# Kernel optimization log

Measured on AMD Instinct MI355X. Metric: run time of the kernel, lower is better.

Reference implementation:

```python
import jax, jax.numpy as jnp
import numpy as np

D_MODEL = 256
N_HEADS = 8
HEAD_DIM = D_MODEL // N_HEADS
EPS = 1e-6


def setup_inputs() -> dict:
    key = jax.random.key(0)
    ks = jax.random.split(key, 12)
    B, L, S = 8, 8192, 8192
    scale = 1.0 / np.sqrt(D_MODEL)
    inp = {
        "queries": jax.random.normal(ks[0], (B, L, D_MODEL), jnp.float32),
        "keys": jax.random.normal(ks[1], (B, S, D_MODEL), jnp.float32),
        "values": jax.random.normal(ks[2], (B, S, D_MODEL), jnp.float32),
        "query_masks": jnp.ones((B, L), jnp.float32),
        "key_masks": jnp.ones((B, S), jnp.float32),
        # nn.Linear params (torch layout: W [out,in], y = x @ W.T + b)
        "Wq": jax.random.normal(ks[3], (D_MODEL, D_MODEL), jnp.float32) * scale,
        "bq": jax.random.normal(ks[4], (D_MODEL,), jnp.float32) * scale,
        "Wk": jax.random.normal(ks[5], (D_MODEL, D_MODEL), jnp.float32) * scale,
        "bk": jax.random.normal(ks[6], (D_MODEL,), jnp.float32) * scale,
        "Wv": jax.random.normal(ks[7], (D_MODEL, D_MODEL), jnp.float32) * scale,
        "bv": jax.random.normal(ks[8], (D_MODEL,), jnp.float32) * scale,
        "Wm": jax.random.normal(ks[9], (D_MODEL, D_MODEL), jnp.float32) * scale,
        "bm": jax.random.normal(ks[10], (D_MODEL,), jnp.float32) * scale,
    }
    return inp


def _feature_map(x):
    return jax.nn.elu(x) + 1.0


def reference(queries, keys, values, query_masks, key_masks,
              Wq, bq, Wk, bk, Wv, bv, Wm, bm):
    B, L, D = queries.shape
    S = keys.shape[1]
    H, hd = N_HEADS, HEAD_DIM

    q = (queries @ Wq.T + bq).reshape(B, L, H, hd)
    k = (keys @ Wk.T + bk).reshape(B, S, H, hd)
    v = (values @ Wv.T + bv).reshape(B, S, H, hd)

    Q = _feature_map(q) * query_masks[:, :, None, None]
    K = _feature_map(k) * key_masks[:, :, None, None]
    v = v * key_masks[:, :, None, None]

    # KV: [B,H,hd_v(m),hd_k(d)]
    KV = jnp.einsum("nshd,nshm->nhmd", K, v)
    Z = 1.0 / (jnp.einsum("nlhd,nhd->nlh", Q, K.sum(axis=1)) + EPS)
    V = jnp.einsum("nlhd,nhmd,nlh->nlhm", Q, KV, Z)
    return V.reshape(B, L, D) @ Wm.T + bm
```

## Files before the change

kernel.cpp:

```cpp
#include <hip/hip_runtime.h>
#include <math.h>


#define B_ 8
#define S_ 8192
#define D_ 256
#define H_ 8
#define EPS_ 1e-6f

typedef short short8 __attribute__((ext_vector_type(8)));
typedef float f32x16 __attribute__((ext_vector_type(16)));

#define KA_K 0
#define KA_V 32768
#define KA_M 65536
#define KA_BYTES 66048
#define KB_Q 0
#define KB_O 32768
#define KB_M 65536
#define KB_S 66048
#define KB_BQ 67072
#define KB_BYTES 68096

static __device__ __forceinline__ unsigned short f2bf(float f) {
  union { float f; unsigned u; } v; v.f = f;
  return (unsigned short)((v.u + 0x7fffu + ((v.u >> 16) & 1u)) >> 16);
}
static __device__ __forceinline__ unsigned pack2(float a, float b) {
  return (unsigned)f2bf(a) | ((unsigned)f2bf(b) << 16);
}

static __device__ __forceinline__ void stage_issue(const float* __restrict__ src,
                                                   int tid, float4* R) {
  const float4* s4 = (const float4*)src;
#pragma unroll
  for (int i = 0; i < 16; ++i) R[i] = s4[i * 256 + tid];
}
static __device__ __forceinline__ void stage_write(char* __restrict__ dst,
                                                   int tid, const float4* R) {
  const int w = tid >> 6, lane = tid & 63, g = lane >> 1, j = lane & 1;
#pragma unroll
  for (int i = 0; i < 16; ++i) {
    const int tok = 4 * i + w;
    *(ushort4*)(dst + ((g * 64 + (tok ^ (g & 31))) * 16 + j * 8)) =
        make_ushort4(f2bf(R[i].x), f2bf(R[i].y), f2bf(R[i].z), f2bf(R[i].w));
  }
}

static __device__ __forceinline__ short8 mk_frag(unsigned w00, unsigned w01,
                                                 unsigned w10, unsigned w11, int kg) {
  unsigned a0 = kg ? w10 : w00, a1 = kg ? w11 : w01;
  unsigned s0 = kg ? w00 : w10, s1 = kg ? w01 : w11;
  unsigned r0 = __shfl_xor(s0, 32), r1 = __shfl_xor(s1, 32);
  union { unsigned u[4]; short8 s8; } f;
  f.u[0] = kg ? r0 : a0; f.u[1] = kg ? r1 : a1;
  f.u[2] = kg ? a0 : r0; f.u[3] = kg ? a1 : r1;
  return f.s8;
}

template <bool XOR>
static __device__ __forceinline__ void gemm_std(const char* __restrict__ ldsX,
                                                const short8* __restrict__ Wf,
                                                int w, int lo, int kg, f32x16 acc[2][2]) {
#pragma unroll
  for (int a = 0; a < 2; ++a)
#pragma unroll
    for (int c = 0; c < 2; ++c)
#pragma unroll
      for (int i = 0; i < 16; ++i) acc[a][c][i] = 0.f;
#pragma unroll 4
  for (int ks = 0; ks < 16; ++ks) {
    const int g = 2 * ks + kg;
    short8 af[2], bf[2];
#pragma unroll
    for (int mt = 0; mt < 2; ++mt) {
      int tok = mt * 32 + lo;
      if (XOR) tok ^= (g & 31);
      af[mt] = *(const short8*)(ldsX + (g * 64 + tok) * 16);
    }
#pragma unroll
    for (int nt = 0; nt < 2; ++nt) bf[nt] = Wf[g * 256 + w * 64 + nt * 32 + lo];
#pragma unroll
    for (int mt = 0; mt < 2; ++mt)
#pragma unroll
      for (int nt = 0; nt < 2; ++nt)
        acc[mt][nt] = __builtin_amdgcn_mfma_f32_32x32x16_bf16(af[mt], bf[nt],
                                                              acc[mt][nt], 0, 0, 0);
  }
}

static __device__ __forceinline__ void gemm_flip(const char* __restrict__ ldsX,
                                                 const short8* __restrict__ Wf,
                                                 int w, int lo, int kg, f32x16 acc[2][2]) {
#pragma unroll
  for (int a = 0; a < 2; ++a)
#pragma unroll
    for (int c = 0; c < 2; ++c)
#pragma unroll
      for (int i = 0; i < 16; ++i) acc[a][c][i] = 0.f;
#pragma unroll 4
  for (int ks = 0; ks < 16; ++ks) {
    const int g = 2 * ks + kg;
    short8 aw[2], bx[2];
#pragma unroll
    for (int At = 0; At < 2; ++At) aw[At] = Wf[g * 256 + w * 64 + At * 32 + lo];
#pragma unroll
    for (int Bt = 0; Bt < 2; ++Bt)
      bx[Bt] = *(const short8*)(ldsX + (g * 64 + ((Bt * 32 + lo) ^ (g & 31))) * 16);
#pragma unroll
    for (int At = 0; At < 2; ++At)
#pragma unroll
      for (int Bt = 0; Bt < 2; ++Bt)
        acc[At][Bt] = __builtin_amdgcn_mfma_f32_32x32x16_bf16(aw[At], bx[Bt],
                                                              acc[At][Bt], 0, 0, 0);
  }
}

__global__ void kPrep(const float* __restrict__ Wq, const float* __restrict__ Wk,
                      const float* __restrict__ Wv, const float* __restrict__ Wm,
                      unsigned short* __restrict__ Wf) {
  int idx = blockIdx.x * 256 + threadIdx.x;
  int wsel = idx >> 13, g = (idx >> 8) & 31, o = idx & 255;
  const float* W = wsel == 0 ? Wq : wsel == 1 ? Wk : wsel == 2 ? Wv : Wm;
  const float* p = W + o * 256 + g * 8;
  *(ushort4*)(Wf + (size_t)idx * 8) =
      make_ushort4(f2bf(p[0]), f2bf(p[1]), f2bf(p[2]), f2bf(p[3]));
  *(ushort4*)(Wf + (size_t)idx * 8 + 4) =
      make_ushort4(f2bf(p[4]), f2bf(p[5]), f2bf(p[6]), f2bf(p[7]));
}

__global__ void __launch_bounds__(256, 2)
kA(const float* __restrict__ keys, const float* __restrict__ values,
   const float* __restrict__ kmask,
   const float* __restrict__ bk, const float* __restrict__ bv,
   const short8* __restrict__ WfK, const short8* __restrict__ WfV,
   float* __restrict__ kvpart, float* __restrict__ kspart,
   float* __restrict__ KV, float* __restrict__ Ksum, int use_atomic) {
  extern __shared__ char lds[];
  char* ldsK = lds + KA_K;
  char* ldsV = lds + KA_V;
  float* ldsM = (float*)(lds + KA_M);
  const int tid = threadIdx.x, w = tid >> 6, lane = tid & 63, lo = lane & 31, kg = lane >> 5;
  const int blk = blockIdx.x, b = blockIdx.y;
  const size_t base = ((size_t)b * S_ + blk * 128) * D_;

  const float bk0 = bk[w * 64 + lo], bk1 = bk[w * 64 + 32 + lo];
  const float bv0 = bv[w * 64 + lo], bv1 = bv[w * 64 + 32 + lo];

  f32x16 kvacc[2];
#pragma unroll
  for (int hh = 0; hh < 2; ++hh)
#pragma unroll
    for (int i = 0; i < 16; ++i) kvacc[hh][i] = 0.f;
  float ks0 = 0.f, ks1 = 0.f;

  float4 RK[16], RV[16];
  stage_issue(keys + base, tid, RK);
  stage_issue(values + base, tid, RV);
  if (tid < 128) ldsM[tid] = kmask[(size_t)b * S_ + blk * 128 + tid];
  stage_write(ldsK, tid, RK);

#pragma unroll
  for (int it = 0; it < 2; ++it) {
    __syncthreads();
    f32x16 acc[2][2];
    gemm_std<true>(ldsK, WfK, w, lo, kg, acc);

    unsigned Wk_[2][2][4][2];
#pragma unroll
    for (int mt = 0; mt < 2; ++mt)
#pragma unroll
      for (int nt = 0; nt < 2; ++nt) {
        const float bias = nt ? bk1 : bk0;
#pragma unroll
        for (int q = 0; q < 4; ++q) {
          float vv[4];
#pragma unroll
          for (int c = 0; c < 4; ++c) {
            const int tok = it * 64 + 32 * mt + 8 * q + 4 * kg + c;
            float f = acc[mt][nt][4 * q + c] + bias;
            f = f > 0.f ? f + 1.f : __expf(f);
            f *= ldsM[tok];
            if (nt == 0) ks0 += f; else ks1 += f;
            vv[c] = f;
          }
          Wk_[mt][nt][q][0] = pack2(vv[0], vv[1]);
          Wk_[mt][nt][q][1] = pack2(vv[2], vv[3]);
        }
      }
    short8 kf[2][4];
#pragma unroll
    for (int nt = 0; nt < 2; ++nt)
#pragma unroll
      for (int mt = 0; mt < 2; ++mt)
#pragma unroll
        for (int sel = 0; sel < 2; ++sel)
          kf[nt][2 * mt + sel] = mk_frag(Wk_[mt][nt][2 * sel][0], Wk_[mt][nt][2 * sel][1],
                                         Wk_[mt][nt][2 * sel + 1][0], Wk_[mt][nt][2 * sel + 1][1], kg);

    stage_write(ldsV, tid, RV);
    if (it == 0) stage_issue(keys + base + 64 * D_, tid, RK);
    __syncthreads();

    gemm_std<true>(ldsV, WfV, w, lo, kg, acc);
    unsigned Wv_[2][2][4][2];
#pragma unroll
    for (int mt = 0; mt < 2; ++mt)
#pragma unroll
      for (int nt = 0; nt < 2; ++nt) {
        const float bias = nt ? bv1 : bv0;
#pragma unroll
        for (int q = 0; q < 4; ++q) {
          float vv[4];
#pragma unroll
          for (int c = 0; c < 4; ++c) {
            const int tok = it * 64 + 32 * mt + 8 * q + 4 * kg + c;
            vv[c] = (acc[mt][nt][4 * q + c] + bias) * ldsM[tok];
          }
          Wv_[mt][nt][q][0] = pack2(vv[0], vv[1]);
          Wv_[mt][nt][q][1] = pack2(vv[2], vv[3]);
        }
      }
    short8 vf[2][4];
#pragma unroll
    for (int nt = 0; nt < 2; ++nt)
#pragma unroll
      for (int mt = 0; mt < 2; ++mt)
#pragma unroll
        for (int sel = 0; sel < 2; ++sel)
          vf[nt][2 * mt + sel] = mk_frag(Wv_[mt][nt][2 * sel][0], Wv_[mt][nt][2 * sel][1],
                                         Wv_[mt][nt][2 * sel + 1][0], Wv_[mt][nt][2 * sel + 1][1], kg);
    if (it == 0) stage_issue(values + base + 64 * D_, tid, RV);

#pragma unroll
    for (int hh = 0; hh < 2; ++hh)
#pragma unroll
      for (int tg = 0; tg < 4; ++tg)
        kvacc[hh] = __builtin_amdgcn_mfma_f32_32x32x16_bf16(kf[hh][tg], vf[hh][tg],
                                                            kvacc[hh], 0, 0, 0);
    if (it == 0) stage_write(ldsK, tid, RK);
  }

  const float tot0 = ks0 + __shfl_xor(ks0, 32);
  const float tot1 = ks1 + __shfl_xor(ks1, 32);
  if (use_atomic) {
    atomicAdd(&Ksum[b * 256 + w * 64 + kg * 32 + lo], kg ? tot1 : tot0);
#pragma unroll
    for (int hh = 0; hh < 2; ++hh) {
      const int h = 2 * w + hh;
#pragma unroll
      for (int r = 0; r < 16; ++r) {
        const int d = (r & 3) + 8 * (r >> 2) + 4 * kg;
        atomicAdd(&KV[(((size_t)b * H_ + h) * 32 + lo) * 32 + d], kvacc[hh][r]);
      }
    }
  } else {
    kspart[((size_t)b * 64 + blk) * 256 + w * 64 + kg * 32 + lo] = kg ? tot1 : tot0;
#pragma unroll
    for (int hh = 0; hh < 2; ++hh) {
      const int h = 2 * w + hh;
      float* dst = kvpart + ((size_t)b * 64 + blk) * 8192 + ((h * 2 + kg) * 16) * 32 + lo;
#pragma unroll
      for (int r = 0; r < 16; ++r) dst[r * 32] = kvacc[hh][r];
    }
  }
}

__global__ void kR(const float* __restrict__ kvpart, const float* __restrict__ kspart,
                   float* __restrict__ KV, float* __restrict__ Ksum) {
  int idx = blockIdx.x * 256 + threadIdx.x;
  if (idx < 65536) {
    int b = idx >> 13, r2 = idx & 8191;
    int h = r2 >> 10, kg2 = (r2 >> 9) & 1, rr = (r2 >> 5) & 15, m = r2 & 31;
    const float* p = kvpart + (size_t)b * 64 * 8192 + r2;
    float s = 0.f;
#pragma unroll 8
    for (int j = 0; j < 64; ++j) s += p[(size_t)j * 8192];
    int d = (rr & 3) + 4 * kg2 + 8 * (rr >> 2);
    KV[(((size_t)b * H_ + h) * 32 + m) * 32 + d] = s;
  } else if (idx < 67584) {
    int t = idx - 65536;
    int b = t >> 8, o = t & 255;
    const float* p = kspart + (size_t)b * 64 * 256 + o;
    float s = 0.f;
#pragma unroll 8
    for (int j = 0; j < 64; ++j) s += p[j * 256];
    Ksum[t] = s;
  }
}

__global__ void __launch_bounds__(256, 2)
kB(const float* __restrict__ queries, const float* __restrict__ qmask,
   const float* __restrict__ bq, const float* __restrict__ bm,
   const short8* __restrict__ WfQ, const short8* __restrict__ WfM,
   const float* __restrict__ KV, const float* __restrict__ Ksum,
   float* __restrict__ out) {
  extern __shared__ char lds[];
  char* ldsQ = lds + KB_Q;
  char* ldsO = lds + KB_O;
  float* ldsM = (float*)(lds + KB_M);
  float* ldsS = (float*)(lds + KB_S);
  float* ldsBq = (float*)(lds + KB_BQ);
  const int tid = threadIdx.x, w = tid >> 6, lane = tid & 63, lo = lane & 31, kg = lane >> 5;
  const int blk = blockIdx.x, b = blockIdx.y;
  const size_t base = ((size_t)b * S_ + blk * 128) * D_;

  ldsS[tid] = Ksum[b * 256 + tid];
  ldsBq[tid] = bq[tid];
  if (tid < 128) ldsM[tid] = qmask[(size_t)b * S_ + blk * 128 + tid];
  const float bm0 = bm[w * 64 + lo], bm1 = bm[w * 64 + 32 + lo];

  short8 kvf[2][2];
#pragma unroll
  for (int hh = 0; hh < 2; ++hh)
#pragma unroll
    for (int ksd = 0; ksd < 2; ++ksd) {
      const float* p = KV + (((size_t)b * H_ + 2 * w + hh) * 32 + lo) * 32 + ksd * 16 + kg * 8;
      float4 x0 = *(const float4*)p, x1 = *(const float4*)(p + 4);
      union { unsigned u[4]; short8 s8; } t;
      t.u[0] = pack2(x0.x, x0.y); t.u[1] = pack2(x0.z, x0.w);
      t.u[2] = pack2(x1.x, x1.y); t.u[3] = pack2(x1.z, x1.w);
      kvf[hh][ksd] = t.s8;
    }

  float4 RQ[16];
  stage_issue(queries + base, tid, RQ);
  stage_write(ldsQ, tid, RQ);

#pragma unroll
  for (int it = 0; it < 2; ++it) {
    __syncthreads();
    f32x16 qa[2][2];
    gemm_flip(ldsQ, WfQ, w, lo, kg, qa);
    if (it == 0) stage_issue(queries + base + 64 * D_, tid, RQ);

    unsigned Wq_[2][2][4][2];
    float inv_[2][2];
#pragma unroll
    for (int At = 0; At < 2; ++At) {
      float kss[4][4], bql[4][4];
#pragma unroll
      for (int q = 0; q < 4; ++q)
#pragma unroll
        for (int c = 0; c < 4; ++c) {
          const int o = w * 64 + At * 32 + 8 * q + 4 * kg + c;
          kss[q][c] = ldsS[o];
          bql[q][c] = ldsBq[o];
        }
#pragma unroll
      for (int Bt = 0; Bt < 2; ++Bt) {
        const float qm = ldsM[it * 64 + Bt * 32 + lo];
        float z = 0.f;
#pragma unroll
        for (int q = 0; q < 4; ++q) {
          float vv[4];
#pragma unroll
          for (int c = 0; c < 4; ++c) {
            float f = qa[At][Bt][4 * q + c] + bql[q][c];
            f = f > 0.f ? f + 1.f : __expf(f);
            f *= qm;
            z += f * kss[q][c];
            vv[c] = f;
          }
          Wq_[At][Bt][q][0] = pack2(vv[0], vv[1]);
          Wq_[At][Bt][q][1] = pack2(vv[2], vv[3]);
        }
        const float zf = z + __shfl_xor(z, 32);
        inv_[At][Bt] = 1.0f / (zf + EPS_);
      }
    }

#pragma unroll
    for (int hh = 0; hh < 2; ++hh) {
      const int h = 2 * w + hh;
#pragma unroll
      for (int Bt = 0; Bt < 2; ++Bt) {
        f32x16 pn;
#pragma unroll
        for (int i = 0; i < 16; ++i) pn[i] = 0.f;
#pragma unroll
        for (int ksd = 0; ksd < 2; ++ksd) {
          short8 qf = mk_frag(Wq_[hh][Bt][2 * ksd][0], Wq_[hh][Bt][2 * ksd][1],
                              Wq_[hh][Bt][2 * ksd + 1][0], Wq_[hh][Bt][2 * ksd + 1][1], kg);
          pn = __builtin_amdgcn_mfma_f32_32x32x16_bf16(kvf[hh][ksd], qf, pn, 0, 0, 0);
        }
        const float inv = inv_[hh][Bt];
        const int tok = Bt * 32 + lo;
#pragma unroll
        for (int q = 0; q < 4; ++q)
          *(ushort4*)(ldsO + ((h * 4 + q) * 64 + tok) * 16 + kg * 8) =
              make_ushort4(f2bf(pn[4 * q + 0] * inv), f2bf(pn[4 * q + 1] * inv),
                           f2bf(pn[4 * q + 2] * inv), f2bf(pn[4 * q + 3] * inv));
      }
    }
    __syncthreads();

    f32x16 oa[2][2];
    gemm_std<false>(ldsO, WfM, w, lo, kg, oa);
    if (it == 0) stage_write(ldsQ, tid, RQ);

    const int t0 = blk * 128 + it * 64;
#pragma unroll
    for (int mt = 0; mt < 2; ++mt)
#pragma unroll
      for (int nt = 0; nt < 2; ++nt) {
        const float bias = nt ? bm1 : bm0;
        const int o = w * 64 + nt * 32 + lo;
        float* dst = out + ((size_t)b * S_ + t0 + 32 * mt) * D_ + o;
#pragma unroll
        for (int r = 0; r < 16; ++r) {
          const int tok = (r & 3) + 8 * (r >> 2) + 4 * kg;
          dst[(size_t)tok * D_] = oa[mt][nt][r] + bias;
        }
      }
  }
}

extern "C" void kernel_launch(void* const* d_in, const int* in_sizes, int n_in,
                              void* d_out, int out_size, void* d_ws, size_t ws_size,
                              hipStream_t stream) {
  const float* queries = (const float*)d_in[0];
  const float* keys    = (const float*)d_in[1];
  const float* values  = (const float*)d_in[2];
  const float* qmask   = (const float*)d_in[3];
  const float* kmask   = (const float*)d_in[4];
  const float* Wq = (const float*)d_in[5];
  const float* bq = (const float*)d_in[6];
  const float* Wk = (const float*)d_in[7];
  const float* bk = (const float*)d_in[8];
  const float* Wv = (const float*)d_in[9];
  const float* bv = (const float*)d_in[10];
  const float* Wm = (const float*)d_in[11];
  const float* bm = (const float*)d_in[12];
  float* out = (float*)d_out;

  char* ws = (char*)d_ws;
  unsigned short* Wf = (unsigned short*)ws;
  float* KV   = (float*)(ws + 524288);
  float* Ksum = (float*)(ws + 786432);
  float* kvpart = (float*)(ws + 1048576);
  float* kspart = (float*)(ws + 1048576 + 16777216);
  const size_t need = 1048576 + 16777216 + 524288;
  const int use_atomic = (ws_size < need) ? 1 : 0;

  hipFuncSetAttribute(reinterpret_cast<const void*>(kA),
                      hipFuncAttributeMaxDynamicSharedMemorySize, KA_BYTES);
  hipFuncSetAttribute(reinterpret_cast<const void*>(kB),
                      hipFuncAttributeMaxDynamicSharedMemorySize, KB_BYTES);

  kPrep<<<128, 256, 0, stream>>>(Wq, Wk, Wv, Wm, Wf);
  if (use_atomic) hipMemsetAsync(ws + 524288, 0, 262144 + 8192, stream);

  const short8* Wf8 = (const short8*)Wf;
  kA<<<dim3(64, B_), 256, KA_BYTES, stream>>>(keys, values, kmask, bk, bv,
      Wf8 + (size_t)1 * 8192, Wf8 + (size_t)2 * 8192, kvpart, kspart, KV, Ksum, use_atomic);
  if (!use_atomic) kR<<<264, 256, 0, stream>>>(kvpart, kspart, KV, Ksum);
  kB<<<dim3(64, B_), 256, KB_BYTES, stream>>>(queries, qmask, bq, bm,
      Wf8, Wf8 + (size_t)3 * 8192, KV, Ksum, out);
}
```

Baseline: 316.8 us.

## Stage fp32 tiles via direct global-to-LDS loads and shrink per-block token tiles

Both projection kernels now load fp32 input rows straight into LDS with global_load_lds into a swizzled layout, then convert to bf16 with v_cvt_pk_bf16_f32 when reading MFMA fragments. This replaces the register-staged load, convert and store path. kA now works on 32-token tiles with a single LDS buffer shared by keys and values over four iterations. kB handles 32 tokens per block with four times as many blocks, and LDS is cut so that three blocks fit per CU. The aim is to save VGPRs and staging instructions and to raise occupancy, at the cost of less prefetch overlap between tiles and smaller MFMA tiles per wave.

After: 370.1 us. 1.17x slower.

```diff
diff --git a/kernel.cpp b/kernel.cpp
--- a/kernel.cpp
+++ b/kernel.cpp
@@ -11,16 +11,15 @@
 typedef short short8 __attribute__((ext_vector_type(8)));
 typedef float f32x16 __attribute__((ext_vector_type(16)));
 
-#define KA_K 0
-#define KA_V 32768
-#define KA_M 65536
-#define KA_BYTES 66048
+#define KA_X 0
+#define KA_M 32768
+#define KA_BYTES 33280
 #define KB_Q 0
 #define KB_O 32768
-#define KB_M 65536
-#define KB_S 66048
-#define KB_BQ 67072
-#define KB_BYTES 68096
+#define KB_M 49152
+#define KB_S 49280
+#define KB_BQ 50304
+#define KB_BYTES 51328
 
 static __device__ __forceinline__ unsigned short f2bf(float f) {
   union { float f; unsigned u; } v; v.f = f;
@@ -29,22 +28,41 @@
 static __device__ __forceinline__ unsigned pack2(float a, float b) {
   return (unsigned)f2bf(a) | ((unsigned)f2bf(b) << 16);
 }
-
-static __device__ __forceinline__ void stage_issue(const float* __restrict__ src,
-                                                   int tid, float4* R) {
-  const float4* s4 = (const float4*)src;
-#pragma unroll
-  for (int i = 0; i < 16; ++i) R[i] = s4[i * 256 + tid];
-}
-static __device__ __forceinline__ void stage_write(char* __restrict__ dst,
-                                                   int tid, const float4* R) {
-  const int w = tid >> 6, lane = tid & 63, g = lane >> 1, j = lane & 1;
-#pragma unroll
-  for (int i = 0; i < 16; ++i) {
-    const int tok = 4 * i + w;
-    *(ushort4*)(dst + ((g * 64 + (tok ^ (g & 31))) * 16 + j * 8)) =
-        make_ushort4(f2bf(R[i].x), f2bf(R[i].y), f2bf(R[i].z), f2bf(R[i].w));
-  }
+static __device__ __forceinline__ unsigned cvt_pk(float a, float b) {
+  unsigned r;
+  asm("v_cvt_pk_bf16_f32 %0, %1, %2" : "=v"(r) : "v"(a), "v"(b));
+  return r;
+}
+
+typedef __attribute__((address_space(1))) const void GV;
+typedef __attribute__((address_space(3))) void LV;
+static __device__ __forceinline__ void gll16(const void* gp, void* lp) {
+  __builtin_amdgcn_global_load_lds((GV*)gp, (LV*)lp, 16, 0, 0);
+}
+
+static __device__ __forceinline__ void issue_tile(const float* __restrict__ src,
+                                                  char* __restrict__ buf,
+                                                  int w, int lane) {
+#pragma unroll
+  for (int i = 0; i < 8; ++i) {
+    const int r = w * 8 + i;
+    const float* gp = src + r * 256 + ((lane ^ (r & 15)) << 2);
+    gll16((const void*)gp, (void*)(buf + r * 1024));
+  }
+}
+
+static __device__ __forceinline__ short8 ld_frag_f32(const char* __restrict__ ldsX,
+                                                     int row, int g) {
+  const int s0 = (g * 2) ^ (row & 15);
+  const int s1 = (g * 2 + 1) ^ (row & 15);
+  float4 a = *(const float4*)(ldsX + row * 1024 + s0 * 16);
+  float4 b = *(const float4*)(ldsX + row * 1024 + s1 * 16);
+  union { unsigned u[4]; short8 s8; } t;
+  t.u[0] = cvt_pk(a.x, a.y);
+  t.u[1] = cvt_pk(a.z, a.w);
+  t.u[2] = cvt_pk(b.x, b.y);
+  t.u[3] = cvt_pk(b.z, b.w);
+  return t.s8;
 }
 
 static __device__ __forceinline__ short8 mk_frag(unsigned w00, unsigned w01,
@@ -56,64 +74,6 @@
   f.u[0] = kg ? r0 : a0; f.u[1] = kg ? r1 : a1;
   f.u[2] = kg ? a0 : r0; f.u[3] = kg ? a1 : r1;
   return f.s8;
-}
-
-template <bool XOR>
-static __device__ __forceinline__ void gemm_std(const char* __restrict__ ldsX,
-                                                const short8* __restrict__ Wf,
-                                                int w, int lo, int kg, f32x16 acc[2][2]) {
-#pragma unroll
-  for (int a = 0; a < 2; ++a)
-#pragma unroll
-    for (int c = 0; c < 2; ++c)
-#pragma unroll
-      for (int i = 0; i < 16; ++i) acc[a][c][i] = 0.f;
-#pragma unroll 4
-  for (int ks = 0; ks < 16; ++ks) {
-    const int g = 2 * ks + kg;
-    short8 af[2], bf[2];
-#pragma unroll
-    for (int mt = 0; mt < 2; ++mt) {
-      int tok = mt * 32 + lo;
-      if (XOR) tok ^= (g & 31);
-      af[mt] = *(const short8*)(ldsX + (g * 64 + tok) * 16);
-    }
-#pragma unroll
-    for (int nt = 0; nt < 2; ++nt) bf[nt] = Wf[g * 256 + w * 64 + nt * 32 + lo];
-#pragma unroll
-    for (int mt = 0; mt < 2; ++mt)
-#pragma unroll
-      for (int nt = 0; nt < 2; ++nt)
-        acc[mt][nt] = __builtin_amdgcn_mfma_f32_32x32x16_bf16(af[mt], bf[nt],
-                                                              acc[mt][nt], 0, 0, 0);
-  }
-}
-
-static __device__ __forceinline__ void gemm_flip(const char* __restrict__ ldsX,
-                                                 const short8* __restrict__ Wf,
-                                                 int w, int lo, int kg, f32x16 acc[2][2]) {
-#pragma unroll
-  for (int a = 0; a < 2; ++a)
-#pragma unroll
-    for (int c = 0; c < 2; ++c)
-#pragma unroll
-      for (int i = 0; i < 16; ++i) acc[a][c][i] = 0.f;
-#pragma unroll 4
-  for (int ks = 0; ks < 16; ++ks) {
-    const int g = 2 * ks + kg;
-    short8 aw[2], bx[2];
-#pragma unroll
-    for (int At = 0; At < 2; ++At) aw[At] = Wf[g * 256 + w * 64 + At * 32 + lo];
-#pragma unroll
-    for (int Bt = 0; Bt < 2; ++Bt)
-      bx[Bt] = *(const short8*)(ldsX + (g * 64 + ((Bt * 32 + lo) ^ (g & 31))) * 16);
-#pragma unroll
-    for (int At = 0; At < 2; ++At)
-#pragma unroll
-      for (int Bt = 0; Bt < 2; ++Bt)
-        acc[At][Bt] = __builtin_amdgcn_mfma_f32_32x32x16_bf16(aw[At], bx[Bt],
-                                                              acc[At][Bt], 0, 0, 0);
-  }
 }
 
 __global__ void kPrep(const float* __restrict__ Wq, const float* __restrict__ Wk,
@@ -129,7 +89,7 @@
       make_ushort4(f2bf(p[4]), f2bf(p[5]), f2bf(p[6]), f2bf(p[7]));
 }
 
-__global__ void __launch_bounds__(256, 2)
+__global__ void __launch_bounds__(256, 3)
 kA(const float* __restrict__ keys, const float* __restrict__ values,
    const float* __restrict__ kmask,
    const float* __restrict__ bk, const float* __restrict__ bv,
@@ -137,8 +97,7 @@
    float* __restrict__ kvpart, float* __restrict__ kspart,
    float* __restrict__ KV, float* __restrict__ Ksum, int use_atomic) {
   extern __shared__ char lds[];
-  char* ldsK = lds + KA_K;
-  char* ldsV = lds + KA_V;
+  char* bufX = lds + KA_X;
   float* ldsM = (float*)(lds + KA_M);
   const int tid = threadIdx.x, w = tid >> 6, lane = tid & 63, lo = lane & 31, kg = lane >> 5;
   const int blk = blockIdx.x, b = blockIdx.y;
@@ -154,91 +113,101 @@
     for (int i = 0; i < 16; ++i) kvacc[hh][i] = 0.f;
   float ks0 = 0.f, ks1 = 0.f;
 
-  float4 RK[16], RV[16];
-  stage_issue(keys + base, tid, RK);
-  stage_issue(values + base, tid, RV);
   if (tid < 128) ldsM[tid] = kmask[(size_t)b * S_ + blk * 128 + tid];
-  stage_write(ldsK, tid, RK);
-
-#pragma unroll
-  for (int it = 0; it < 2; ++it) {
+  issue_tile(keys + base, bufX, w, lane);
+
+#pragma unroll 1
+  for (int it = 0; it < 4; ++it) {
     __syncthreads();
-    f32x16 acc[2][2];
-    gemm_std<true>(ldsK, WfK, w, lo, kg, acc);
-
-    unsigned Wk_[2][2][4][2];
-#pragma unroll
-    for (int mt = 0; mt < 2; ++mt)
-#pragma unroll
-      for (int nt = 0; nt < 2; ++nt) {
-        const float bias = nt ? bk1 : bk0;
-#pragma unroll
-        for (int q = 0; q < 4; ++q) {
-          float vv[4];
-#pragma unroll
-          for (int c = 0; c < 4; ++c) {
-            const int tok = it * 64 + 32 * mt + 8 * q + 4 * kg + c;
-            float f = acc[mt][nt][4 * q + c] + bias;
-            f = f > 0.f ? f + 1.f : __expf(f);
-            f *= ldsM[tok];
-            if (nt == 0) ks0 += f; else ks1 += f;
-            vv[c] = f;
-          }
-          Wk_[mt][nt][q][0] = pack2(vv[0], vv[1]);
-          Wk_[mt][nt][q][1] = pack2(vv[2], vv[3]);
+
+    f32x16 acc[2];
+#pragma unroll
+    for (int nt = 0; nt < 2; ++nt)
+#pragma unroll
+      for (int i = 0; i < 16; ++i) acc[nt][i] = 0.f;
+#pragma unroll 4
+    for (int ks = 0; ks < 16; ++ks) {
+      const int g = 2 * ks + kg;
+      short8 af = ld_frag_f32(bufX, lo, g);
+      short8 b0 = WfK[g * 256 + w * 64 + lo];
+      short8 b1 = WfK[g * 256 + w * 64 + 32 + lo];
+      acc[0] = __builtin_amdgcn_mfma_f32_32x32x16_bf16(af, b0, acc[0], 0, 0, 0);
+      acc[1] = __builtin_amdgcn_mfma_f32_32x32x16_bf16(af, b1, acc[1], 0, 0, 0);
+    }
+    __syncthreads();
+    issue_tile(values + base + (size_t)it * 32 * D_, bufX, w, lane);
+
+    unsigned Wk_[2][4][2];
+#pragma unroll
+    for (int nt = 0; nt < 2; ++nt) {
+      const float bias = nt ? bk1 : bk0;
+#pragma unroll
+      for (int q = 0; q < 4; ++q) {
+        float vv[4];
+#pragma unroll
+        for (int c = 0; c < 4; ++c) {
+          const int tok = 8 * q + 4 * kg + c;
+          float f = acc[nt][4 * q + c] + bias;
+          f = f > 0.f ? f + 1.f : __expf(f);
+          f *= ldsM[it * 32 + tok];
+          if (nt == 0) ks0 += f; else ks1 += f;
+          vv[c] = f;
         }
+        Wk_[nt][q][0] = pack2(vv[0], vv[1]);
+        Wk_[nt][q][1] = pack2(vv[2], vv[3]);
       }
-    short8 kf[2][4];
+    }
+    short8 kf[2][2];
 #pragma unroll
     for (int nt = 0; nt < 2; ++nt)
 #pragma unroll
-      for (int mt = 0; mt < 2; ++mt)
-#pragma unroll
-        for (int sel = 0; sel < 2; ++sel)
-          kf[nt][2 * mt + sel] = mk_frag(Wk_[mt][nt][2 * sel][0], Wk_[mt][nt][2 * sel][1],
-                                         Wk_[mt][nt][2 * sel + 1][0], Wk_[mt][nt][2 * sel + 1][1], kg);
-
-    stage_write(ldsV, tid, RV);
-    if (it == 0) stage_issue(keys + base + 64 * D_, tid, RK);
+      for (int sel = 0; sel < 2; ++sel)
+        kf[nt][sel] = mk_frag(Wk_[nt][2 * sel][0], Wk_[nt][2 * sel][1],
+                              Wk_[nt][2 * sel + 1][0], Wk_[nt][2 * sel + 1][1], kg);
+
     __syncthreads();
 
-    gemm_std<true>(ldsV, WfV, w, lo, kg, acc);
-    unsigned Wv_[2][2][4][2];
-#pragma unroll
-    for (int mt = 0; mt < 2; ++mt)
-#pragma unroll
-      for (int nt = 0; nt < 2; ++nt) {
-        const float bias = nt ? bv1 : bv0;
-#pragma unroll
-        for (int q = 0; q < 4; ++q) {
-          float vv[4];
-#pragma unroll
-          for (int c = 0; c < 4; ++c) {
-            const int tok = it * 64 + 32 * mt + 8 * q + 4 * kg + c;
-            vv[c] = (acc[mt][nt][4 * q + c] + bias) * ldsM[tok];
-          }
-          Wv_[mt][nt][q][0] = pack2(vv[0], vv[1]);
-          Wv_[mt][nt][q][1] = pack2(vv[2], vv[3]);
+#pragma unroll
+    for (int nt = 0; nt < 2; ++nt)
+#pragma unroll
+      for (int i = 0; i < 16; ++i) acc[nt][i] = 0.f;
+#pragma unroll 4
+    for (int ks = 0; ks < 16; ++ks) {
+      const int g = 2 * ks + kg;
+      short8 af = ld_frag_f32(bufX, lo, g);
+      short8 b0 = WfV[g * 256 + w * 64 + lo];
+      short8 b1 = WfV[g * 256 + w * 64 + 32 + lo];
+      acc[0] = __builtin_amdgcn_mfma_f32_32x32x16_bf16(af, b0, acc[0], 0, 0, 0);
+      acc[1] = __builtin_amdgcn_mfma_f32_32x32x16_bf16(af, b1, acc[1], 0, 0, 0);
+    }
+    __syncthreads();
+    if (it < 3) issue_tile(keys + base + (size_t)(it + 1) * 32 * D_, bufX, w, lane);
+
+    unsigned Wv_[2][4][2];
+#pragma unroll
+    for (int nt = 0; nt < 2; ++nt) {
+      const float bias = nt ? bv1 : bv0;
+#pragma unroll
+      for (int q = 0; q < 4; ++q) {
+        float vv[4];
+#pragma unroll
+        for (int c = 0; c < 4; ++c) {
+          const int tok = 8 * q + 4 * kg + c;
+          vv[c] = (acc[nt][4 * q + c] + bias) * ldsM[it * 32 + tok];
         }
+        Wv_[nt][q][0] = pack2(vv[0], vv[1]);
+        Wv_[nt][q][1] = pack2(vv[2], vv[3]);
       }
-    short8 vf[2][4];
-#pragma unroll
-    for (int nt = 0; nt < 2; ++nt)
-#pragma unroll
-      for (int mt = 0; mt < 2; ++mt)
-#pragma unroll
-        for (int sel = 0; sel < 2; ++sel)
-          vf[nt][2 * mt + sel] = mk_frag(Wv_[mt][nt][2 * sel][0], Wv_[mt][nt][2 * sel][1],
-                                         Wv_[mt][nt][2 * sel + 1][0], Wv_[mt][nt][2 * sel + 1][1], kg);
-    if (it == 0) stage_issue(values + base + 64 * D_, tid, RV);
-
+    }
 #pragma unroll
     for (int hh = 0; hh < 2; ++hh)
 #pragma unroll
-      for (int tg = 0; tg < 4; ++tg)
-        kvacc[hh] = __builtin_amdgcn_mfma_f32_32x32x16_bf16(kf[hh][tg], vf[hh][tg],
+      for (int sel = 0; sel < 2; ++sel) {
+        short8 vf = mk_frag(Wv_[hh][2 * sel][0], Wv_[hh][2 * sel][1],
+                            Wv_[hh][2 * sel + 1][0], Wv_[hh][2 * sel + 1][1], kg);
+        kvacc[hh] = __builtin_amdgcn_mfma_f32_32x32x16_bf16(kf[hh][sel], vf,
                                                             kvacc[hh], 0, 0, 0);
-    if (it == 0) stage_write(ldsK, tid, RK);
+      }
   }
 
   const float tot0 = ks0 + __shfl_xor(ks0, 32);
@@ -289,25 +258,27 @@
   }
 }
 
-__global__ void __launch_bounds__(256, 2)
+__global__ void __launch_bounds__(256, 3)
 kB(const float* __restrict__ queries, const float* __restrict__ qmask,
    const float* __restrict__ bq, const float* __restrict__ bm,
    const short8* __restrict__ WfQ, const short8* __restrict__ WfM,
    const float* __restrict__ KV, const float* __restrict__ Ksum,
    float* __restrict__ out) {
   extern __shared__ char lds[];
-  char* ldsQ = lds + KB_Q;
+  char* bufQ = lds + KB_Q;
   char* ldsO = lds + KB_O;
   float* ldsM = (float*)(lds + KB_M);
   float* ldsS = (float*)(lds + KB_S);
   float* ldsBq = (float*)(lds + KB_BQ);
   const int tid = threadIdx.x, w = tid >> 6, lane = tid & 63, lo = lane & 31, kg = lane >> 5;
   const int blk = blockIdx.x, b = blockIdx.y;
-  const size_t base = ((size_t)b * S_ + blk * 128) * D_;
+  const size_t base = ((size_t)b * S_ + blk * 32) * D_;
+
+  issue_tile(queries + base, bufQ, w, lane);
 
   ldsS[tid] = Ksum[b * 256 + tid];
   ldsBq[tid] = bq[tid];
-  if (tid < 128) ldsM[tid] = qmask[(size_t)b * S_ + blk * 128 + tid];
+  if (tid < 32) ldsM[tid] = qmask[(size_t)b * S_ + blk * 32 + tid];
   const float bm0 = bm[w * 64 + lo], bm1 = bm[w * 64 + 32 + lo];
 
   short8 kvf[2][2];
@@ -323,96 +294,93 @@
       kvf[hh][ksd] = t.s8;
     }
 
-  float4 RQ[16];
-  stage_issue(queries + base, tid, RQ);
-  stage_write(ldsQ, tid, RQ);
-
-#pragma unroll
-  for (int it = 0; it < 2; ++it) {
-    __syncthreads();
-    f32x16 qa[2][2];
-    gemm_flip(ldsQ, WfQ, w, lo, kg, qa);
-    if (it == 0) stage_issue(queries + base + 64 * D_, tid, RQ);
-
-    unsigned Wq_[2][2][4][2];
-    float inv_[2][2];
-#pragma unroll
-    for (int At = 0; At < 2; ++At) {
-      float kss[4][4], bql[4][4];
-#pragma unroll
-      for (int q = 0; q < 4; ++q)
-#pragma unroll
-        for (int c = 0; c < 4; ++c) {
-          const int o = w * 64 + At * 32 + 8 * q + 4 * kg + c;
-          kss[q][c] = ldsS[o];
-          bql[q][c] = ldsBq[o];
-        }
-#pragma unroll
-      for (int Bt = 0; Bt < 2; ++Bt) {
-        const float qm = ldsM[it * 64 + Bt * 32 + lo];
-        float z = 0.f;
-#pragma unroll
-        for (int q = 0; q < 4; ++q) {
-          float vv[4];
-#pragma unroll
-          for (int c = 0; c < 4; ++c) {
-            float f = qa[At][Bt][4 * q + c] + bql[q][c];
-            f = f > 0.f ? f + 1.f : __expf(f);
-            f *= qm;
-            z += f * kss[q][c];
-            vv[c] = f;
-          }
-          Wq_[At][Bt][q][0] = pack2(vv[0], vv[1]);
-          Wq_[At][Bt][q][1] = pack2(vv[2], vv[3]);
-        }
-        const float zf = z + __shfl_xor(z, 32);
-        inv_[At][Bt] = 1.0f / (zf + EPS_);
+  __syncthreads();
+
+  f32x16 qa[2];
+#pragma unroll
+  for (int At = 0; At < 2; ++At)
+#pragma unroll
+    for (int i = 0; i < 16; ++i) qa[At][i] = 0.f;
+#pragma unroll 4
+  for (int ks = 0; ks < 16; ++ks) {
+    const int g = 2 * ks + kg;
+    short8 a0 = WfQ[g * 256 + w * 64 + lo];
+    short8 a1 = WfQ[g * 256 + w * 64 + 32 + lo];
+    short8 bx = ld_frag_f32(bufQ, lo, g);
+    qa[0] = __builtin_amdgcn_mfma_f32_32x32x16_bf16(a0, bx, qa[0], 0, 0, 0);
+    qa[1] = __builtin_amdgcn_mfma_f32_32x32x16_bf16(a1, bx, qa[1], 0, 0, 0);
+  }
+
+  unsigned Wq_[2][4][2];
+  float inv_[2];
+  const float qm = ldsM[lo];
+#pragma unroll
+  for (int At = 0; At < 2; ++At) {
+    float z = 0.f;
+#pragma unroll
+    for (int q = 0; q < 4; ++q) {
+      float vv[4];
+#pragma unroll
+      for (int c = 0; c < 4; ++c) {
+        const int o = w * 64 + At * 32 + 8 * q + 4 * kg + c;
+        float f = qa[At][4 * q + c] + ldsBq[o];
+        f = f > 0.f ? f + 1.f : __expf(f);
+        f *= qm;
+        z += f * ldsS[o];
+        vv[c] = f;
       }
-    }
-
-#pragma unroll
-    for (int hh = 0; hh < 2; ++hh) {
-      const int h = 2 * w + hh;
-#pragma unroll
-      for (int Bt = 0; Bt < 2; ++Bt) {
-        f32x16 pn;
-#pragma unroll
-        for (int i = 0; i < 16; ++i) pn[i] = 0.f;
-#pragma unroll
-        for (int ksd = 0; ksd < 2; ++ksd) {
-          short8 qf = mk_frag(Wq_[hh][Bt][2 * ksd][0], Wq_[hh][Bt][2 * ksd][1],
-                              Wq_[hh][Bt][2 * ksd + 1][0], Wq_[hh][Bt][2 * ksd + 1][1], kg);
-          pn = __builtin_amdgcn_mfma_f32_32x32x16_bf16(kvf[hh][ksd], qf, pn, 0, 0, 0);
-        }
-        const float inv = inv_[hh][Bt];
-        const int tok = Bt * 32 + lo;
-#pragma unroll
-        for (int q = 0; q < 4; ++q)
-          *(ushort4*)(ldsO + ((h * 4 + q) * 64 + tok) * 16 + kg * 8) =
-              make_ushort4(f2bf(pn[4 * q + 0] * inv), f2bf(pn[4 * q + 1] * inv),
-                           f2bf(pn[4 * q + 2] * inv), f2bf(pn[4 * q + 3] * inv));
-      }
-    }
-    __syncthreads();
-
-    f32x16 oa[2][2];
-    gemm_std<false>(ldsO, WfM, w, lo, kg, oa);
-    if (it == 0) stage_write(ldsQ, tid, RQ);
-
-    const int t0 = blk * 128 + it * 64;
-#pragma unroll
-    for (int mt = 0; mt < 2; ++mt)
-#pragma unroll
-      for (int nt = 0; nt < 2; ++nt) {
-        const float bias = nt ? bm1 : bm0;
-        const int o = w * 64 + nt * 32 + lo;
-        float* dst = out + ((size_t)b * S_ + t0 + 32 * mt) * D_ + o;
-#pragma unroll
-        for (int r = 0; r < 16; ++r) {
-          const int tok = (r & 3) + 8 * (r >> 2) + 4 * kg;
-          dst[(size_t)tok * D_] = oa[mt][nt][r] + bias;
-        }
-      }
+      Wq_[At][q][0] = pack2(vv[0], vv[1]);
+      Wq_[At][q][1] = pack2(vv[2], vv[3]);
+    }
+    const float zf = z + __shfl_xor(z, 32);
+    inv_[At] = 1.0f / (zf + EPS_);
+  }
+
+#pragma unroll
+  for (int hh = 0; hh < 2; ++hh) {
+    const int h = 2 * w + hh;
+    f32x16 pn;
+#pragma unroll
+    for (int i = 0; i < 16; ++i) pn[i] = 0.f;
+#pragma unroll
+    for (int ksd = 0; ksd < 2; ++ksd) {
+      short8 qf = mk_frag(Wq_[hh][2 * ksd][0], Wq_[hh][2 * ksd][1],
+                          Wq_[hh][2 * ksd + 1][0], Wq_[hh][2 * ksd + 1][1], kg);
+      pn = __builtin_amdgcn_mfma_f32_32x32x16_bf16(kvf[hh][ksd], qf, pn, 0, 0, 0);
+    }
+    const float inv = inv_[hh];
+#pragma unroll
+    for (int q = 0; q < 4; ++q)
+      *(ushort4*)(ldsO + ((h * 4 + q) * 32 + lo) * 16 + kg * 8) =
+          make_ushort4(f2bf(pn[4 * q + 0] * inv), f2bf(pn[4 * q + 1] * inv),
+                       f2bf(pn[4 * q + 2] * inv), f2bf(pn[4 * q + 3] * inv));
+  }
+  __syncthreads();
+
+  f32x16 oa[2];
+#pragma unroll
+  for (int nt = 0; nt < 2; ++nt)
+#pragma unroll
+    for (int i = 0; i < 16; ++i) oa[nt][i] = 0.f;
+#pragma unroll 4
+  for (int ks = 0; ks < 16; ++ks) {
+    const int g = 2 * ks + kg;
+    short8 av = *(const short8*)(ldsO + (g * 32 + lo) * 16);
+    short8 b0 = WfM[g * 256 + w * 64 + lo];
+    short8 b1 = WfM[g * 256 + w * 64 + 32 + lo];
+    oa[0] = __builtin_amdgcn_mfma_f32_32x32x16_bf16(av, b0, oa[0], 0, 0, 0);
+    oa[1] = __builtin_amdgcn_mfma_f32_32x32x16_bf16(av, b1, oa[1], 0, 0, 0);
+  }
+#pragma unroll
+  for (int nt = 0; nt < 2; ++nt) {
+    const float bias = nt ? bm1 : bm0;
+    const int o = w * 64 + nt * 32 + lo;
+    float* dst = out + ((size_t)b * S_ + blk * 32) * D_ + o;
+#pragma unroll
+    for (int r = 0; r < 16; ++r) {
+      const int tok = (r & 3) + 8 * (r >> 2) + 4 * kg;
+      dst[(size_t)tok * D_] = oa[nt][r] + bias;
+    }
   }
 }
 
@@ -443,18 +411,18 @@
   const size_t need = 1048576 + 16777216 + 524288;
   const int use_atomic = (ws_size < need) ? 1 : 0;
 
-  hipFuncSetAttribute(reinterpret_cast<const void*>(kA),
-                      hipFuncAttributeMaxDynamicSharedMemorySize, KA_BYTES);
-  hipFuncSetAttribute(reinterpret_cast<const void*>(kB),
-                      hipFuncAttributeMaxDynamicSharedMemorySize, KB_BYTES);
+  (void)hipFuncSetAttribute(reinterpret_cast<const void*>(kA),
+                            hipFuncAttributeMaxDynamicSharedMemorySize, KA_BYTES);
+  (void)hipFuncSetAttribute(reinterpret_cast<const void*>(kB),
+                            hipFuncAttributeMaxDynamicSharedMemorySize, KB_BYTES);
 
   kPrep<<<128, 256, 0, stream>>>(Wq, Wk, Wv, Wm, Wf);
-  if (use_atomic) hipMemsetAsync(ws + 524288, 0, 262144 + 8192, stream);
+  if (use_atomic) (void)hipMemsetAsync(ws + 524288, 0, 262144 + 8192, stream);
 
   const short8* Wf8 = (const short8*)Wf;
   kA<<<dim3(64, B_), 256, KA_BYTES, stream>>>(keys, values, kmask, bk, bv,
       Wf8 + (size_t)1 * 8192, Wf8 + (size_t)2 * 8192, kvpart, kspart, KV, Ksum, use_atomic);
   if (!use_atomic) kR<<<264, 256, 0, stream>>>(kvpart, kspart, KV, Ksum);
-  kB<<<dim3(64, B_), 256, KB_BYTES, stream>>>(queries, qmask, bq, bm,
+  kB<<<dim3(256, B_), 256, KB_BYTES, stream>>>(queries, qmask, bq, bm,
       Wf8, Wf8 + (size_t)3 * 8192, KV, Ksum, out);
 }
```
